# Kernel optimization log

Hardware: AMD Instinct MI355X
Metric: run time of the kernel (lower is better)

The kernel has to match this reference:

```python
import jax, jax.numpy as jnp
import numpy as np

VOCAB, EMB, HID = 128000, 128, 1024
B, S = 4, 4096

def setup_inputs() -> dict:
    key = jax.random.key(0)
    k1, k2, k3 = jax.random.split(key, 3)
    x = jax.random.randint(k1, (B, S), 0, VOCAB, dtype=jnp.int64)
    embed_vocab = jax.random.normal(k2, (VOCAB, EMB), dtype=jnp.float32)
    embed_hidden = jax.random.normal(k3, (EMB, HID), dtype=jnp.float32)
    return {"x": x, "embed_vocab": embed_vocab, "embed_hidden": embed_hidden}

def reference(x, embed_vocab, embed_hidden):
    # Faithful to the torch module: build the full factorized table [V,H]
    # then gather rows by token id (F.embedding with defaults: no padding_idx,
    # no max_norm).
    table = embed_vocab @ embed_hidden          # [V, H]
    return jnp.take(table, x, axis=0)           # [B, S, H]
```

## Files before the change

### kernel.cpp

```cpp
#include <hip/hip_runtime.h>


using f32x4 = __attribute__((ext_vector_type(4))) float;
using i32x4 = __attribute__((ext_vector_type(4))) int;

constexpr int EMB = 128;
constexpr int HID = 1024;

__device__ inline void cvt8(const float f[8], i32x4& hi, i32x4& lo) {
    unsigned h[8], l[8];
#pragma unroll
    for (int e = 0; e < 8; ++e) {
        unsigned fb = __float_as_uint(f[e]);
        unsigned hb = fb & 0xFFFF0000u;
        float r = f[e] - __uint_as_float(hb);
        unsigned lb = __float_as_uint(r) & 0xFFFF0000u;
        h[e] = hb; l[e] = lb;
    }
#pragma unroll
    for (int p = 0; p < 4; ++p) {
        hi[p] = (int)((h[2*p] >> 16) | h[2*p+1]);
        lo[p] = (int)((l[2*p] >> 16) | l[2*p+1]);
    }
}

__device__ inline f32x4 mfma_bf16(i32x4 a, i32x4 b, f32x4 c) {
    f32x4 d;
    asm volatile("v_mfma_f32_16x16x32_bf16 %0, %1, %2, %3"
                 : "=v"(d) : "v"(a), "v"(b), "0"(c));
    return d;
}

__global__ __launch_bounds__(256, 2)
void femb_mfma(const int* __restrict__ x,
               const float* __restrict__ ev,
               const float* __restrict__ eh,
               float* __restrict__ out, int mtiles)
{
    __shared__ __align__(16) char lds[65536];
    char* Ah = lds;
    char* Al = lds + 16384;
    char* Bh = lds + 32768;
    char* Bl = lds + 49152;

    const int tid  = threadIdx.x;
    const int bid  = blockIdx.x;
    const int mt   = bid % mtiles;
    const int nt   = bid / mtiles;
    const long m0  = (long)mt * 128;
    const long n0  = (long)nt * 128;
    const int lane = tid & 63;
    const int wid  = tid >> 6;
    const int wm   = wid >> 1, wn = wid & 1;
    const int rl   = lane & 15, g = lane >> 4;

    f32x4 acc[4][4];
#pragma unroll
    for (int i = 0; i < 4; ++i)
#pragma unroll
        for (int j = 0; j < 4; ++j) acc[i][j] = (f32x4){0.f, 0.f, 0.f, 0.f};

    for (int h = 0; h < 2; ++h) {
        if (h) __syncthreads();

#pragma unroll
        for (int i = 0; i < 4; ++i) {
            const int c   = tid + 256 * i;
            const int tok = c >> 3, k8 = c & 7;
            const long id = x[m0 + tok];
            const float* src = ev + id * EMB + h * 64 + k8 * 8;
            float f[8];
            *(float4*)(f)     = *(const float4*)(src);
            *(float4*)(f + 4) = *(const float4*)(src + 4);
            i32x4 hi, lo; cvt8(f, hi, lo);
            const int off = tok * 128 + ((k8 * 16) ^ ((tok & 7) << 4));
            *(i32x4*)(Ah + off) = hi;
            *(i32x4*)(Al + off) = lo;
        }
#pragma unroll
        for (int i = 0; i < 4; ++i) {
            const int c  = tid + 256 * i;
            const int n  = c & 127, k8 = c >> 7;
            float f[8];
#pragma unroll
            for (int j = 0; j < 8; ++j)
                f[j] = eh[(long)(h * 64 + k8 * 8 + j) * HID + n0 + n];
            i32x4 hi, lo; cvt8(f, hi, lo);
            const int off = n * 128 + ((k8 * 16) ^ ((n & 7) << 4));
            *(i32x4*)(Bh + off) = hi;
            *(i32x4*)(Bl + off) = lo;
        }
        __syncthreads();

#pragma unroll
        for (int kk = 0; kk < 2; ++kk) {
            i32x4 a_h[4], a_l[4], b_h[4], b_l[4];
#pragma unroll
            for (int mf = 0; mf < 4; ++mf) {
                const int row = wm * 64 + mf * 16 + rl;
                const int off = row * 128 + ((kk * 64 + g * 16) ^ ((row & 7) << 4));
                a_h[mf] = *(const i32x4*)(Ah + off);
                a_l[mf] = *(const i32x4*)(Al + off);
            }
#pragma unroll
            for (int nf = 0; nf < 4; ++nf) {
                const int nr  = wn * 64 + nf * 16 + rl;
                const int off = nr * 128 + ((kk * 64 + g * 16) ^ ((nr & 7) << 4));
                b_h[nf] = *(const i32x4*)(Bh + off);
                b_l[nf] = *(const i32x4*)(Bl + off);
            }
#pragma unroll
            for (int mf = 0; mf < 4; ++mf)
#pragma unroll
                for (int nf = 0; nf < 4; ++nf) {
                    acc[mf][nf] = mfma_bf16(a_h[mf], b_h[nf], acc[mf][nf]);
                    acc[mf][nf] = mfma_bf16(a_h[mf], b_l[nf], acc[mf][nf]);
                    acc[mf][nf] = mfma_bf16(a_l[mf], b_h[nf], acc[mf][nf]);
                }
        }
    }

#pragma unroll
    for (int mf = 0; mf < 4; ++mf)
#pragma unroll
        for (int j = 0; j < 4; ++j) {
            const long row = m0 + wm * 64 + mf * 16 + g * 4 + j;
            float* dst = out + row * HID + n0 + wn * 64 + rl;
#pragma unroll
            for (int nf = 0; nf < 4; ++nf) dst[nf * 16] = acc[mf][nf][j];
        }
}

extern "C" void kernel_launch(void* const* d_in, const int* in_sizes, int n_in,
                              void* d_out, int out_size, void* d_ws, size_t ws_size,
                              hipStream_t stream) {
    const int*   x   = (const int*)d_in[0];
    const float* ev  = (const float*)d_in[1];
    const float* eh  = (const float*)d_in[2];
    float*       out = (float*)d_out;

    const int M      = in_sizes[0];
    const int mtiles = M / 128;
    const int grid   = mtiles * (HID / 128);
    femb_mfma<<<grid, 256, 0, stream>>>(x, ev, eh, out, mtiles);
}
```

Before: 121.6 us.

## Precompute bf16 hi/lo splits in workspace and stream tiles with async LDS loads

Adds two prep kernels that gather token rows and convert both operands into split bf16 hi/lo form once, stored in a swizzled workspace layout. The main kernel then fills LDS with global_load_lds DMA over four double-buffered K stages instead of converting in every tile. This removes the work of redoing the gather and conversion eight times per token row (once per N tile) and overlaps loads with MFMA. In exchange it adds two extra launches and a workspace round trip for the A operand.

```diff
diff --git a/kernel.cpp b/kernel.cpp
--- a/kernel.cpp
+++ b/kernel.cpp
@@ -3,18 +3,19 @@
 
 using f32x4 = __attribute__((ext_vector_type(4))) float;
 using i32x4 = __attribute__((ext_vector_type(4))) int;
+typedef unsigned int u32;
 
 constexpr int EMB = 128;
 constexpr int HID = 1024;
 
 __device__ inline void cvt8(const float f[8], i32x4& hi, i32x4& lo) {
-    unsigned h[8], l[8];
+    u32 h[8], l[8];
 #pragma unroll
     for (int e = 0; e < 8; ++e) {
-        unsigned fb = __float_as_uint(f[e]);
-        unsigned hb = fb & 0xFFFF0000u;
+        u32 fb = __float_as_uint(f[e]);
+        u32 hb = fb & 0xFFFF0000u;
         float r = f[e] - __uint_as_float(hb);
-        unsigned lb = __float_as_uint(r) & 0xFFFF0000u;
+        u32 lb = __float_as_uint(r) & 0xFFFF0000u;
         h[e] = hb; l[e] = lb;
     }
 #pragma unroll
@@ -27,32 +28,64 @@
 __device__ inline f32x4 mfma_bf16(i32x4 a, i32x4 b, f32x4 c) {
     f32x4 d;
     asm volatile("v_mfma_f32_16x16x32_bf16 %0, %1, %2, %3"
-                 : "=v"(d) : "v"(a), "v"(b), "0"(c));
+                 : "=&v"(d) : "v"(a), "v"(b), "v"(c));
     return d;
 }
 
+__device__ inline void gload16(const u32* src, u32* ldsdst) {
+    __builtin_amdgcn_global_load_lds(
+        (const __attribute__((address_space(1))) u32*)src,
+        (__attribute__((address_space(3))) u32*)ldsdst, 16, 0, 0);
+}
+
+__global__ void prep_eh(const float* __restrict__ eh, u32* __restrict__ wsBh,
+                        u32* __restrict__ wsBl) {
+    const int t  = blockIdx.x * 256 + threadIdx.x;
+    const int n  = t >> 4, k8 = t & 15;
+    float f[8];
+#pragma unroll
+    for (int j = 0; j < 8; ++j) f[j] = eh[(k8*8 + j)*HID + n];
+    i32x4 hi, lo; cvt8(f, hi, lo);
+    const int s = k8 >> 2, gs = (k8 & 3) ^ ((n >> 1) & 3);
+    const int off = (s*HID + n)*16 + gs*4;
+    *(i32x4*)(wsBh + off) = hi;
+    *(i32x4*)(wsBl + off) = lo;
+}
+
+__global__ void prep_ev(const int* __restrict__ x, const float* __restrict__ ev,
+                        u32* __restrict__ wsAh, u32* __restrict__ wsAl, int M) {
+    const int t = blockIdx.x * 256 + threadIdx.x;
+    const int m = t >> 4, k8 = t & 15;
+    const long id = x[m];
+    const float* src = ev + id * EMB + k8*8;
+    float f[8];
+    *(float4*)(f)     = *(const float4*)(src);
+    *(float4*)(f + 4) = *(const float4*)(src + 4);
+    i32x4 hi, lo; cvt8(f, hi, lo);
+    const int s = k8 >> 2, gs = (k8 & 3) ^ ((m >> 1) & 3);
+    const long off = ((long)s*M + m)*16 + gs*4;
+    *(i32x4*)(wsAh + off) = hi;
+    *(i32x4*)(wsAl + off) = lo;
+}
+
 __global__ __launch_bounds__(256, 2)
-void femb_mfma(const int* __restrict__ x,
-               const float* __restrict__ ev,
-               const float* __restrict__ eh,
-               float* __restrict__ out, int mtiles)
+void femb_main(const u32* __restrict__ wsAh, const u32* __restrict__ wsAl,
+               const u32* __restrict__ wsBh, const u32* __restrict__ wsBl,
+               float* __restrict__ out, int mtiles, int M)
 {
-    __shared__ __align__(16) char lds[65536];
-    char* Ah = lds;
-    char* Al = lds + 16384;
-    char* Bh = lds + 32768;
-    char* Bl = lds + 49152;
+    __shared__ __align__(16) u32 lds[2][4][2048];
 
     const int tid  = threadIdx.x;
+    const int lane = tid & 63, wid = tid >> 6;
     const int bid  = blockIdx.x;
     const int mt   = bid % mtiles;
     const int nt   = bid / mtiles;
-    const long m0  = (long)mt * 128;
-    const long n0  = (long)nt * 128;
-    const int lane = tid & 63;
-    const int wid  = tid >> 6;
+    const long m0  = (long)mt * 128, n0 = (long)nt * 128;
     const int wm   = wid >> 1, wn = wid & 1;
     const int rl   = lane & 15, g = lane >> 4;
+
+    const int row_ = wid*32 + (lane >> 2);
+    const int gr_  = lane & 3;
 
     f32x4 acc[4][4];
 #pragma unroll
@@ -60,72 +93,58 @@
 #pragma unroll
         for (int j = 0; j < 4; ++j) acc[i][j] = (f32x4){0.f, 0.f, 0.f, 0.f};
 
-    for (int h = 0; h < 2; ++h) {
-        if (h) __syncthreads();
+    auto stage = [&](int s, int buf) {
+#pragma unroll
+        for (int j = 0; j < 2; ++j) {
+            const int  r  = row_ + j*16;
+            const int  lo = wid*512 + j*256;
+            const long ao = ((long)s*M   + m0 + r)*16 + gr_*4;
+            const long bo = ((long)s*HID + n0 + r)*16 + gr_*4;
+            gload16(wsAh + ao, &lds[buf][0][lo]);
+            gload16(wsAl + ao, &lds[buf][1][lo]);
+            gload16(wsBh + bo, &lds[buf][2][lo]);
+            gload16(wsBl + bo, &lds[buf][3][lo]);
+        }
+    };
 
+    auto compute = [&](int buf) {
+        i32x4 bh[4], bl[4];
 #pragma unroll
-        for (int i = 0; i < 4; ++i) {
-            const int c   = tid + 256 * i;
-            const int tok = c >> 3, k8 = c & 7;
-            const long id = x[m0 + tok];
-            const float* src = ev + id * EMB + h * 64 + k8 * 8;
-            float f[8];
-            *(float4*)(f)     = *(const float4*)(src);
-            *(float4*)(f + 4) = *(const float4*)(src + 4);
-            i32x4 hi, lo; cvt8(f, hi, lo);
-            const int off = tok * 128 + ((k8 * 16) ^ ((tok & 7) << 4));
-            *(i32x4*)(Ah + off) = hi;
-            *(i32x4*)(Al + off) = lo;
+        for (int nf = 0; nf < 4; ++nf) {
+            const int nr  = wn*64 + nf*16 + rl;
+            const int off = nr*16 + ((g ^ ((nr >> 1) & 3)) << 2);
+            bh[nf] = *(const i32x4*)&lds[buf][2][off];
+            bl[nf] = *(const i32x4*)&lds[buf][3][off];
         }
 #pragma unroll
-        for (int i = 0; i < 4; ++i) {
-            const int c  = tid + 256 * i;
-            const int n  = c & 127, k8 = c >> 7;
-            float f[8];
-#pragma unroll
-            for (int j = 0; j < 8; ++j)
-                f[j] = eh[(long)(h * 64 + k8 * 8 + j) * HID + n0 + n];
-            i32x4 hi, lo; cvt8(f, hi, lo);
-            const int off = n * 128 + ((k8 * 16) ^ ((n & 7) << 4));
-            *(i32x4*)(Bh + off) = hi;
-            *(i32x4*)(Bl + off) = lo;
-        }
-        __syncthreads();
-
-#pragma unroll
-        for (int kk = 0; kk < 2; ++kk) {
-            i32x4 a_h[4], a_l[4], b_h[4], b_l[4];
-#pragma unroll
-            for (int mf = 0; mf < 4; ++mf) {
-                const int row = wm * 64 + mf * 16 + rl;
-                const int off = row * 128 + ((kk * 64 + g * 16) ^ ((row & 7) << 4));
-                a_h[mf] = *(const i32x4*)(Ah + off);
-                a_l[mf] = *(const i32x4*)(Al + off);
-            }
+        for (int mf = 0; mf < 4; ++mf) {
+            const int mr  = wm*64 + mf*16 + rl;
+            const int off = mr*16 + ((g ^ ((mr >> 1) & 3)) << 2);
+            const i32x4 ah = *(const i32x4*)&lds[buf][0][off];
+            const i32x4 al = *(const i32x4*)&lds[buf][1][off];
 #pragma unroll
             for (int nf = 0; nf < 4; ++nf) {
-                const int nr  = wn * 64 + nf * 16 + rl;
-                const int off = nr * 128 + ((kk * 64 + g * 16) ^ ((nr & 7) << 4));
-                b_h[nf] = *(const i32x4*)(Bh + off);
-                b_l[nf] = *(const i32x4*)(Bl + off);
+                acc[mf][nf] = mfma_bf16(ah, bh[nf], acc[mf][nf]);
+                acc[mf][nf] = mfma_bf16(ah, bl[nf], acc[mf][nf]);
+                acc[mf][nf] = mfma_bf16(al, bh[nf], acc[mf][nf]);
             }
-#pragma unroll
-            for (int mf = 0; mf < 4; ++mf)
-#pragma unroll
-                for (int nf = 0; nf < 4; ++nf) {
-                    acc[mf][nf] = mfma_bf16(a_h[mf], b_h[nf], acc[mf][nf]);
-                    acc[mf][nf] = mfma_bf16(a_h[mf], b_l[nf], acc[mf][nf]);
-                    acc[mf][nf] = mfma_bf16(a_l[mf], b_h[nf], acc[mf][nf]);
-                }
         }
+    };
+
+    stage(0, 0);
+    for (int s = 0; s < 4; ++s) {
+        __builtin_amdgcn_s_waitcnt(0);
+        __syncthreads();
+        if (s < 3) stage(s + 1, (s + 1) & 1);
+        compute(s & 1);
     }
 
 #pragma unroll
     for (int mf = 0; mf < 4; ++mf)
 #pragma unroll
         for (int j = 0; j < 4; ++j) {
-            const long row = m0 + wm * 64 + mf * 16 + g * 4 + j;
-            float* dst = out + row * HID + n0 + wn * 64 + rl;
+            const long row = m0 + wm*64 + mf*16 + g*4 + j;
+            float* dst = out + row * HID + n0 + wn*64 + rl;
 #pragma unroll
             for (int nf = 0; nf < 4; ++nf) dst[nf * 16] = acc[mf][nf][j];
         }
@@ -141,6 +160,15 @@
 
     const int M      = in_sizes[0];
     const int mtiles = M / 128;
-    const int grid   = mtiles * (HID / 128);
-    femb_mfma<<<grid, 256, 0, stream>>>(x, ev, eh, out, mtiles);
+
+    u32* wsBh = (u32*)d_ws;
+    u32* wsBl = wsBh + (size_t)HID*64;
+    u32* wsAh = wsBl + (size_t)HID*64;
+    u32* wsAl = wsAh + (size_t)M*64;
+    if (ws_size < (size_t)(2*HID*64 + 2*(size_t)M*64) * 4) return;
+
+    prep_eh<<<HID*16/256, 256, 0, stream>>>(eh, wsBh, wsBl);
+    prep_ev<<<M*16/256, 256, 0, stream>>>(x, ev, wsAh, wsAl, M);
+    femb_main<<<mtiles * (HID/128), 256, 0, stream>>>(wsAh, wsAl, wsBh, wsBl,
+                                                      out, mtiles, M);
 }
```

New measurement: 123.6 us. About the same (+1.7%).
